# Kernel tuning notes

Hardware: AMD Instinct MI355X
Metric: run time of the kernel (lower is better)

## Reference

```python
import jax, jax.numpy as jnp
import numpy as np

B, S, E, F, R, T = 2, 2048, 768, 3072, 4, 128
H = 12  # num_heads
HD = E // H
HID = 128  # lora_mlp_dim


def _lin(key, out_f, in_f):
    bound = 1.0 / np.sqrt(in_f)
    return jax.random.uniform(key, (out_f, in_f), jnp.float32, -bound, bound)


def _bias(key, out_f, in_f):
    bound = 1.0 / np.sqrt(in_f)
    return jax.random.uniform(key, (out_f,), jnp.float32, -bound, bound)


def setup_inputs() -> dict:
    key = jax.random.key(0)
    ks = jax.random.split(key, 20)
    return {
        "src": jax.random.normal(ks[0], (B, S, E), jnp.float32),
        "task_embedding": jax.random.normal(ks[1], (B, S, T), jnp.float32),
        "norm1_w": jnp.ones((E,), jnp.float32),
        "norm2_w": jnp.ones((E,), jnp.float32),
        "in_proj_w": _lin(ks[2], 3 * E, E),      # MHA qkv, bias=False
        "out_proj_w": _lin(ks[3], E, E),          # MHA out, bias=False
        "ffn1_w": _lin(ks[4], F, E), "ffn1_b": _bias(ks[5], F, E),
        "ffn2_w": _lin(ks[6], E, F), "ffn2_b": _bias(ks[7], E, F),
        "hA_w1": _lin(ks[8], HID, T), "hA_b1": _bias(ks[9], HID, T),
        "hA_w2": _lin(ks[10], F * R, HID), "hA_b2": _bias(ks[11], F * R, HID),
        "hB_w1": _lin(ks[12], HID, T), "hB_b1": _bias(ks[13], HID, T),
        "hB_w2": _lin(ks[14], R * E, HID), "hB_b2": _bias(ks[15], R * E, HID),
    }


def _rmsnorm(x, w):
    eps = jnp.finfo(x.dtype).eps
    return x * jax.lax.rsqrt(jnp.mean(x * x, axis=-1, keepdims=True) + eps) * w


def reference(src, task_embedding, norm1_w, norm2_w, in_proj_w, out_proj_w,
              ffn1_w, ffn1_b, ffn2_w, ffn2_b,
              hA_w1, hA_b1, hA_w2, hA_b2, hB_w1, hB_b1, hB_w2, hB_b2):
    # --- self-attention block (pre-RMSNorm) ---
    x = _rmsnorm(src, norm1_w)
    qkv = jnp.einsum('bse,fe->bsf', x, in_proj_w)  # [B,S,3E]
    q, k, v = jnp.split(qkv, 3, axis=-1)
    q = q.reshape(B, S, H, HD).transpose(0, 2, 1, 3)
    k = k.reshape(B, S, H, HD).transpose(0, 2, 1, 3)
    v = v.reshape(B, S, H, HD).transpose(0, 2, 1, 3)
    scores = jnp.einsum('bhqd,bhkd->bhqk', q, k) / jnp.sqrt(jnp.float32(HD))
    attn = jax.nn.softmax(scores, axis=-1)
    ctx = jnp.einsum('bhqk,bhkd->bhqd', attn, v)
    ctx = ctx.transpose(0, 2, 1, 3).reshape(B, S, E)
    attn_out = jnp.einsum('bse,fe->bsf', ctx, out_proj_w)
    src = src + attn_out

    # --- FFN block with per-token hypernetwork LoRA on linear1 ---
    x = _rmsnorm(src, norm2_w)
    # hypernetwork: MLP(task) -> per-token A [F,R], B [R,E]
    hA = jax.nn.relu(jnp.einsum('bst,ht->bsh', task_embedding, hA_w1) + hA_b1)
    A_params = (jnp.einsum('bsh,fh->bsf', hA, hA_w2) + hA_b2).reshape(B, S, F, R)
    hB = jax.nn.relu(jnp.einsum('bst,ht->bsh', task_embedding, hB_w1) + hB_b1)
    B_params = (jnp.einsum('bsh,fh->bsf', hB, hB_w2) + hB_b2).reshape(B, S, R, E)

    base = jnp.einsum('bse,fe->bsf', x, ffn1_w) + ffn1_b  # [B,S,F]
    inter = jnp.einsum('bse,bsre->bsr', x, B_params)       # [B,S,R]
    adapt = jnp.einsum('bsr,bsfr->bsf', inter, A_params)   # [B,S,F]
    h = jax.nn.relu(base + adapt)
    out2 = jnp.einsum('bsf,ef->bse', h, ffn2_w) + ffn2_b
    return src + out2
```

## Files before the change

### kernel.cpp

```cpp
#include <hip/hip_runtime.h>
#include <math.h>

#define NB 2
#define NS 2048
#define NE 768
#define NF 3072
#define NHEAD 12
#define NTOK 4096
#define LDW 1344
#define VTS 2176

typedef __bf16 bf16;
typedef __bf16 bf16x2 __attribute__((ext_vector_type(2)));
typedef __bf16 bf16x4 __attribute__((ext_vector_type(4)));
typedef __bf16 bf16x8 __attribute__((ext_vector_type(8)));
typedef float  f32x4  __attribute__((ext_vector_type(4)));

__device__ __forceinline__ f32x4 mfma_bf16(bf16x8 a, bf16x8 b, f32x4 c) {
  return __builtin_amdgcn_mfma_f32_16x16x32_bf16(a, b, c, 0, 0, 0);
}

__device__ __forceinline__ float fast_exp2(float x) {
#if __has_builtin(__builtin_amdgcn_exp2f)
  return __builtin_amdgcn_exp2f(x);
#else
  return exp2f(x);
#endif
}

__device__ __forceinline__ void glds16(const void* g, void* l) {
  __builtin_amdgcn_global_load_lds((const __attribute__((address_space(1))) void*)g,
                                   (__attribute__((address_space(3))) void*)l,
                                   16, 0, 0);
}

__device__ __forceinline__ void pipe_barrier_keep4() {
  asm volatile("s_waitcnt vmcnt(4)" ::: "memory");
  __builtin_amdgcn_s_barrier();
  __builtin_amdgcn_sched_barrier(0);
}
__device__ __forceinline__ void pipe_barrier_drain() {
  asm volatile("s_waitcnt vmcnt(0)" ::: "memory");
  __builtin_amdgcn_s_barrier();
  __builtin_amdgcn_sched_barrier(0);
}

__device__ __forceinline__ void swz_xy(int& bx, int& by) {
  int gx = gridDim.x;
  int i = by*gx + bx;
  int xcd = i & 7, s = i >> 3;
  int bands = gridDim.y >> 3;
  by = xcd*bands + s / gx;
  bx = s % gx;
}

__global__ void prep_kernel(const float* __restrict__ in_proj, const float* __restrict__ out_proj,
                            const float* __restrict__ ffn1_w, const float* __restrict__ ffn1_b,
                            const float* __restrict__ ffn2_w,
                            const float* __restrict__ hA_w1, const float* __restrict__ hA_b1,
                            const float* __restrict__ hA_w2, const float* __restrict__ hA_b2,
                            const float* __restrict__ hB_w1, const float* __restrict__ hB_b1,
                            const float* __restrict__ hB_w2,
                            const float* __restrict__ task,
                            bf16* __restrict__ Wqkv, bf16* __restrict__ Wo, bf16* __restrict__ W2,
                            bf16* __restrict__ W1ab, float* __restrict__ b1ab,
                            bf16* __restrict__ WBp, bf16* __restrict__ Wc,
                            bf16* __restrict__ task_bf)
{
  __shared__ float tb[64*130];
  int stride = gridDim.x * blockDim.x;
  int t0 = blockIdx.x * blockDim.x + threadIdx.x;
  const float QS = 0.125f * 1.44269504088896f;
  for (int i = t0; i < (2304*768)/4; i += stride) {
    float4 v = ((const float4*)in_proj)[i];
    float sc = (i < (768*768)/4) ? QS : 1.0f;
    *(bf16x4*)(Wqkv + i*4) = (bf16x4){(bf16)(v.x*sc), (bf16)(v.y*sc), (bf16)(v.z*sc), (bf16)(v.w*sc)};
  }
  for (int i = t0; i < (768*768)/4; i += stride) {
    float4 v = ((const float4*)out_proj)[i];
    *(bf16x4*)(Wo + i*4) = (bf16x4){(bf16)v.x, (bf16)v.y, (bf16)v.z, (bf16)v.w};
  }
  for (int i = t0; i < (768*3072)/4; i += stride) {
    float4 v = ((const float4*)ffn2_w)[i];
    *(bf16x4*)(W2 + i*4) = (bf16x4){(bf16)v.x, (bf16)v.y, (bf16)v.z, (bf16)v.w};
  }
  for (int i = t0; i < (NTOK*128)/4; i += stride) {
    float4 v = ((const float4*)task)[i];
    *(bf16x4*)(task_bf + i*4) = (bf16x4){(bf16)v.x, (bf16)v.y, (bf16)v.z, (bf16)v.w};
  }
  for (int i = t0; i < 256*128;  i += stride)
    W1ab[i] = (bf16)(i < 128*128 ? hA_w1[i] : hB_w1[i - 128*128]);
  for (int i = t0; i < 256; i += stride) b1ab[i] = (i < 128) ? hA_b1[i] : hB_b1[i-128];

  for (int j0 = blockIdx.x*64; j0 < 3072; j0 += gridDim.x*64) {
    __syncthreads();
    for (int i = threadIdx.x; i < 64*128; i += 256) {
      int jr = i >> 7, hh = i & 127;
      tb[jr*130 + hh] = hB_w2[(long)(j0 + jr)*128 + hh];
    }
    __syncthreads();
    int r = j0 / 768, e0 = j0 % 768;
    for (int i = threadIdx.x; i < 128*64; i += 256) {
      int hh = i >> 6, jr = i & 63;
      WBp[(long)(r*128 + hh)*768 + e0 + jr] = (bf16)tb[jr*130 + hh];
    }
  }

  for (int f = blockIdx.x; f < 3072; f += gridDim.x) {
    const float* hrow = hA_w2 + (long)f*512;
    bf16* wrow = Wc + (long)f*LDW;
    for (int c = threadIdx.x; c < 768; c += 256) wrow[c] = (bf16)ffn1_w[(long)f*768 + c];
    for (int i = threadIdx.x; i < 512; i += 256) {
      int r = i >> 7, h = i & 127;
      wrow[768 + h*4 + r] = (bf16)hrow[i];
    }
    if (threadIdx.x < 4)        wrow[1280 + threadIdx.x] = (bf16)hA_b2[f*4 + threadIdx.x];
    else if (threadIdx.x == 4)  wrow[1284] = (bf16)ffn1_b[f];
    else if (threadIdx.x < 64)  wrow[1280 + threadIdx.x] = (bf16)0.f;
  }
}

__global__ __launch_bounds__(256) void rmsnorm_k(const float* __restrict__ x,
                                                 const float* __restrict__ w,
                                                 bf16* __restrict__ out, int ld_out)
{
  __shared__ float red[4];
  long t = blockIdx.x;
  const float* xr = x + t*NE;
  float ss = 0.f;
  #pragma unroll
  for (int i = 0; i < 3; i++) { float v = xr[threadIdx.x + i*256]; ss += v*v; }
  #pragma unroll
  for (int d = 1; d < 64; d <<= 1) ss += __shfl_xor(ss, d, 64);
  if ((threadIdx.x & 63) == 0) red[threadIdx.x >> 6] = ss;
  __syncthreads();
  float tot = red[0] + red[1] + red[2] + red[3];
  float scale = rsqrtf(tot * (1.f/768.f) + 1.1920928955078125e-07f);
  #pragma unroll
  for (int i = 0; i < 3; i++) {
    int idx = threadIdx.x + i*256;
    out[t*ld_out + idx] = (bf16)(xr[idx] * scale * w[idx]);
  }
}

__global__ __launch_bounds__(256, 2) void gemm_ph(const bf16* __restrict__ A,
                                                  const bf16* __restrict__ Bm,
                                                  bf16* __restrict__ C,
                                                  int nt, int lda, int ldb, int ldc)
{
  __shared__ bf16 As[2][2][128*32];
  __shared__ bf16 Bs[2][2][192*32];
  const int tid = threadIdx.x;
  int bx = blockIdx.x, by = blockIdx.y;
  swz_xy(bx, by);
  const int m0 = by * 128, n0 = bx * 192;
  const int w = tid >> 6, lane = tid & 63;
  const int quad = lane >> 4, l16 = lane & 15;
  const int wm = w >> 1, wn = w & 1;

  f32x4 acc[4][6];
  #pragma unroll
  for (int i = 0; i < 4; i++)
    #pragma unroll
    for (int j = 0; j < 6; j++) acc[i][j] = (f32x4){0.f,0.f,0.f,0.f};

  const int iA0 = tid,      RA0 = iA0 >> 3, cA0 = (iA0 & 7) ^ (RA0 & 7);
  const int iA1 = tid + 256,RA1 = iA1 >> 3, cA1 = (iA1 & 7) ^ (RA1 & 7);
  const int iB2 = tid + 512,RB2 = iB2 >> 3, cB2 = (iB2 & 7) ^ (RB2 & 7);
  const int rA0 = 2*RA0 + (cA0 >> 2), hA0c = (cA0 & 3)*8;
  const int rA1 = 2*RA1 + (cA1 >> 2), hA1c = (cA1 & 3)*8;
  const int rB2 = 2*RB2 + (cB2 >> 2), hB2c = (cB2 & 3)*8;
  const bf16* paA0 = A  + (long)(m0 + rA0)*lda + hA0c;
  const bf16* paA1 = A  + (long)(m0 + rA1)*lda + hA1c;
  const bf16* pbB0 = Bm + (long)(n0 + rA0)*ldb + hA0c;
  const bf16* pbB1 = Bm + (long)(n0 + rA1)*ldb + hA1c;
  const bf16* pbB2 = Bm + (long)(n0 + rB2)*ldb + hB2c;

  auto stageA = [&](int buf, int kh, int kt) {
    const int s = kt + kh*32;
    glds16(paA0 + s, (void*)(&As[buf][kh][tid*8]));
    glds16(paA1 + s, (void*)(&As[buf][kh][(tid + 256)*8]));
  };
  auto stageB = [&](int buf, int kh, int kt) {
    const int s = kt + kh*32;
    glds16(pbB0 + s, (void*)(&Bs[buf][kh][tid*8]));
    glds16(pbB1 + s, (void*)(&Bs[buf][kh][(tid + 256)*8]));
    glds16(pbB2 + s, (void*)(&Bs[buf][kh][(tid + 512)*8]));
  };

  const int Rh = l16 >> 1;
  const int jfr = (((l16 & 1) << 2) | quad) ^ Rh;
  const int aBase = wm*32, bBase = wn*48;

  auto barrier = [] { __builtin_amdgcn_s_barrier(); __builtin_amdgcn_sched_barrier(0); };

  stageA(0, 0, 0); stageB(0, 0, 0); stageA(0, 1, 0); stageB(0, 1, 0);
  asm volatile("s_waitcnt vmcnt(5)" ::: "memory");
  barrier();

  for (int t = 0; t < nt; ++t) {
    const int cur = t & 1, nb = cur ^ 1;
    const bool more = (t + 1 < nt);
    const int kt1 = (t + 1) << 6;
    bf16x8 af[2], bfr[6];

    #pragma unroll
    for (int j = 0; j < 2; ++j)
      af[j] = *(const bf16x8*)(&As[cur][0][(aBase + j*8 + Rh)*64 + jfr*8]);
    #pragma unroll
    for (int ni = 0; ni < 6; ++ni)
      bfr[ni] = *(const bf16x8*)(&Bs[cur][0][(bBase + ni*8 + Rh)*64 + jfr*8]);
    if (more) stageA(nb, 0, kt1);
    barrier();
    __builtin_amdgcn_s_setprio(1);
    #pragma unroll
    for (int j = 0; j < 2; ++j)
      #pragma unroll
      for (int ni = 0; ni < 6; ++ni)
        acc[j][ni] = mfma_bf16(af[j], bfr[ni], acc[j][ni]);
    __builtin_amdgcn_s_setprio(0);
    barrier();

    #pragma unroll
    for (int j = 0; j < 2; ++j)
      af[j] = *(const bf16x8*)(&As[cur][0][(aBase + 16 + j*8 + Rh)*64 + jfr*8]);
    if (more) stageB(nb, 0, kt1);
    barrier();
    __builtin_amdgcn_s_setprio(1);
    #pragma unroll
    for (int j = 0; j < 2; ++j)
      #pragma unroll
      for (int ni = 0; ni < 6; ++ni)
        acc[2 + j][ni] = mfma_bf16(af[j], bfr[ni], acc[2 + j][ni]);
    __builtin_amdgcn_s_setprio(0);
    if (more) asm volatile("s_waitcnt vmcnt(5)" ::: "memory");
    else      asm volatile("s_waitcnt vmcnt(0)" ::: "memory");
    barrier();

    #pragma unroll
    for (int j = 0; j < 2; ++j)
      af[j] = *(const bf16x8*)(&As[cur][1][(aBase + j*8 + Rh)*64 + jfr*8]);
    #pragma unroll
    for (int ni = 0; ni < 6; ++ni)
      bfr[ni] = *(const bf16x8*)(&Bs[cur][1][(bBase + ni*8 + Rh)*64 + jfr*8]);
    if (more) stageA(nb, 1, kt1);
    barrier();
    __builtin_amdgcn_s_setprio(1);
    #pragma unroll
    for (int j = 0; j < 2; ++j)
      #pragma unroll
      for (int ni = 0; ni < 6; ++ni)
        acc[j][ni] = mfma_bf16(af[j], bfr[ni], acc[j][ni]);
    __builtin_amdgcn_s_setprio(0);
    barrier();

    #pragma unroll
    for (int j = 0; j < 2; ++j)
      af[j] = *(const bf16x8*)(&As[cur][1][(aBase + 16 + j*8 + Rh)*64 + jfr*8]);
    if (more) stageB(nb, 1, kt1);
    barrier();
    __builtin_amdgcn_s_setprio(1);
    #pragma unroll
    for (int j = 0; j < 2; ++j)
      #pragma unroll
      for (int ni = 0; ni < 6; ++ni)
        acc[2 + j][ni] = mfma_bf16(af[j], bfr[ni], acc[2 + j][ni]);
    __builtin_amdgcn_s_setprio(0);
    if (more) asm volatile("s_waitcnt vmcnt(5)" ::: "memory");
    barrier();
  }

  #pragma unroll
  for (int mi = 0; mi < 4; ++mi)
    #pragma unroll
    for (int ni = 0; ni < 6; ++ni) {
      int col = n0 + wn*96 + ni*16 + l16;
      #pragma unroll
      for (int r = 0; r < 4; ++r) {
        long row = m0 + wm*64 + mi*16 + quad*4 + r;
        float v = acc[mi][ni][r];
        C[row*ldc + col] = (bf16)(v > 0.f ? v : 0.f);
      }
    }
}

template<typename OutT, bool RELU, bool BIAS, bool RES>
__global__ __launch_bounds__(256) void gemm64(const bf16* __restrict__ A,
                                              const bf16* __restrict__ Bm,
                                              OutT* __restrict__ C,
                                              const float* __restrict__ bias,
                                              const float* __restrict__ res,
                                              int K, int lda, int ldb, int ldc)
{
  __shared__ bf16 As[3][64*64];
  __shared__ bf16 Bs[3][64*64];
  const int tid = threadIdx.x;
  int bx = blockIdx.x, by = blockIdx.y;
  swz_xy(bx, by);
  const int m0 = by * 64, n0 = bx * 64;
  const int w = tid >> 6, lane = tid & 63;
  const int quad = lane >> 4, l16 = lane & 15;
  const int wy = w >> 1, wx = w & 1;
  const int sw = l16 & 7;

  f32x4 acc[2][2];
  #pragma unroll
  for (int i = 0; i < 2; i++)
    #pragma unroll
    for (int j = 0; j < 2; j++) acc[i][j] = (f32x4){0.f,0.f,0.f,0.f};

  const int c0 = tid, c1 = tid + 256;
  const int r0 = c0 >> 3, g0 = ((c0 & 7) ^ (r0 & 7)) * 8;
  const int r1 = c1 >> 3, g1 = ((c1 & 7) ^ (r1 & 7)) * 8;
  const bf16* pA0 = A  + (long)(m0 + r0)*lda + g0;
  const bf16* pA1 = A  + (long)(m0 + r1)*lda + g1;
  const bf16* pB0 = Bm + (long)(n0 + r0)*ldb + g0;
  const bf16* pB1 = Bm + (long)(n0 + r1)*ldb + g1;
  auto stage = [&](int buf) {
    glds16(pA0, (void*)(&As[buf][c0*8]));
    glds16(pA1, (void*)(&As[buf][c1*8]));
    glds16(pB0, (void*)(&Bs[buf][c0*8]));
    glds16(pB1, (void*)(&Bs[buf][c1*8]));
    pA0 += 64; pA1 += 64; pB0 += 64; pB1 += 64;
  };

  const int nsteps = K >> 6;
  stage(0);
  if (nsteps > 1) stage(1);
  pipe_barrier_keep4();

  int cur = 0, nx2 = 2;
  for (int s = 0; s < nsteps; ++s) {
    const bool more = (s + 2 < nsteps);
    if (more) stage(nx2);

    bf16x8 af[2][2], bfr[2][2];
    #pragma unroll
    for (int mi = 0; mi < 2; ++mi)
      #pragma unroll
      for (int kb = 0; kb < 2; ++kb)
        af[mi][kb] = *(const bf16x8*)(&As[cur][(wy*32 + mi*16 + l16)*64 + (((kb*4 + quad) ^ sw))*8]);
    #pragma unroll
    for (int ni = 0; ni < 2; ++ni)
      #pragma unroll
      for (int kb = 0; kb < 2; ++kb)
        bfr[ni][kb] = *(const bf16x8*)(&Bs[cur][(wx*32 + ni*16 + l16)*64 + (((kb*4 + quad) ^ sw))*8]);
    #pragma unroll
    for (int kb = 0; kb < 2; ++kb)
      #pragma unroll
      for (int mi = 0; mi < 2; ++mi)
        #pragma unroll
        for (int ni = 0; ni < 2; ++ni)
          acc[mi][ni] = mfma_bf16(af[mi][kb], bfr[ni][kb], acc[mi][ni]);

    if (more) pipe_barrier_keep4();
    else      pipe_barrier_drain();
    cur = (cur == 2) ? 0 : cur + 1;
    nx2 = (nx2 == 2) ? 0 : nx2 + 1;
  }

  #pragma unroll
  for (int mi = 0; mi < 2; ++mi)
    #pragma unroll
    for (int ni = 0; ni < 2; ++ni) {
      int col = n0 + wx*32 + ni*16 + l16;
      #pragma unroll
      for (int r = 0; r < 4; ++r) {
        long row = m0 + wy*32 + mi*16 + quad*4 + r;
        float v = acc[mi][ni][r];
        if (BIAS) v += bias[col];
        if (RES)  v += res[row*ldc + col];
        if (RELU) v = v > 0.f ? v : 0.f;
        C[row*ldc + col] = (OutT)v;
      }
    }
}

__global__ __launch_bounds__(256) void gemm_qkv64(const bf16* __restrict__ A,
                                                  const bf16* __restrict__ Bm,
                                                  bf16* __restrict__ Qkv,
                                                  bf16* __restrict__ Vt)
{
  __shared__ bf16 As[3][64*64];
  __shared__ bf16 Bs[3][64*64];
  const int tid = threadIdx.x;
  int bx = blockIdx.x, by = blockIdx.y;
  swz_xy(bx, by);
  const int m0 = by * 64, n0 = bx * 64;
  const int w = tid >> 6, lane = tid & 63;
  const int quad = lane >> 4, l16 = lane & 15;
  const int wy = w >> 1, wx = w & 1;
  const int sw = l16 & 7;

  f32x4 acc[2][2];
  #pragma unroll
  for (int i = 0; i < 2; i++)
    #pragma unroll
    for (int j = 0; j < 2; j++) acc[i][j] = (f32x4){0.f,0.f,0.f,0.f};

  const int c0 = tid, c1 = tid + 256;
  const int r0 = c0 >> 3, g0 = ((c0 & 7) ^ (r0 & 7)) * 8;
  const int r1 = c1 >> 3, g1 = ((c1 & 7) ^ (r1 & 7)) * 8;
  const bf16* pA0 = A  + (long)(m0 + r0)*768 + g0;
  const bf16* pA1 = A  + (long)(m0 + r1)*768 + g1;
  const bf16* pB0 = Bm + (long)(n0 + r0)*768 + g0;
  const bf16* pB1 = Bm + (long)(n0 + r1)*768 + g1;
  auto stage = [&](int buf) {
    glds16(pA0, (void*)(&As[buf][c0*8]));
    glds16(pA1, (void*)(&As[buf][c1*8]));
    glds16(pB0, (void*)(&Bs[buf][c0*8]));
    glds16(pB1, (void*)(&Bs[buf][c1*8]));
    pA0 += 64; pA1 += 64; pB0 += 64; pB1 += 64;
  };

  stage(0);
  stage(1);
  pipe_barrier_keep4();

  int cur = 0, nx2 = 2;
  for (int s = 0; s < 12; ++s) {
    const bool more = (s + 2 < 12);
    if (more) stage(nx2);

    bf16x8 af[2][2], bfr[2][2];
    #pragma unroll
    for (int mi = 0; mi < 2; ++mi)
      #pragma unroll
      for (int kb = 0; kb < 2; ++kb)
        af[mi][kb] = *(const bf16x8*)(&As[cur][(wy*32 + mi*16 + l16)*64 + (((kb*4 + quad) ^ sw))*8]);
    #pragma unroll
    for (int ni = 0; ni < 2; ++ni)
      #pragma unroll
      for (int kb = 0; kb < 2; ++kb)
        bfr[ni][kb] = *(const bf16x8*)(&Bs[cur][(wx*32 + ni*16 + l16)*64 + (((kb*4 + quad) ^ sw))*8]);
    #pragma unroll
    for (int kb = 0; kb < 2; ++kb)
      #pragma unroll
      for (int mi = 0; mi < 2; ++mi)
        #pragma unroll
        for (int ni = 0; ni < 2; ++ni)
          acc[mi][ni] = mfma_bf16(af[mi][kb], bfr[ni][kb], acc[mi][ni]);

    if (more) pipe_barrier_keep4();
    else      pipe_barrier_drain();
    cur = (cur == 2) ? 0 : cur + 1;
    nx2 = (nx2 == 2) ? 0 : nx2 + 1;
  }

  const int bb = m0 >> 11;
  #pragma unroll
  for (int mi = 0; mi < 2; ++mi)
    #pragma unroll
    for (int ni = 0; ni < 2; ++ni) {
      int col = n0 + wx*32 + ni*16 + l16;
      #pragma unroll
      for (int r = 0; r < 4; ++r) {
        long row = m0 + wy*32 + mi*16 + quad*4 + r;
        bf16 v = (bf16)acc[mi][ni][r];
        if (col < 1536) {
          Qkv[row*2304 + col] = v;
        } else {
          int vc = col - 1536;
          int hh = vc >> 6, d = vc & 63;
          long srow = row & (NS-1);
          Vt[((long)(bb*NHEAD + hh)*64 + d)*VTS + srow] = v;
        }
      }
    }
}

__global__ __launch_bounds__(256, 2) void flash_attn(const bf16* __restrict__ Qkv,
                                                     const bf16* __restrict__ Vt,
                                                     bf16* __restrict__ Ctx)
{
  __shared__ bf16 Ks[2][2][64*64];
  __shared__ bf16 Vs[2][2][64*64];

  const int tid = threadIdx.x;
  const int w = tid >> 6, lane = tid & 63;
  const int quad = lane >> 4, l16 = lane & 15;
  const int pair = w >> 1, qw = w & 1;
  int bx = blockIdx.x, by = blockIdx.y;
  swz_xy(bx, by);
  const int bh = by;
  const int b = bh / NHEAD, h = bh % NHEAD;
  const int q0 = bx * 64;

  bf16x8 qf[2][2];
  #pragma unroll
  for (int mi = 0; mi < 2; ++mi) {
    const long tq = (long)(b*NS + q0 + qw*32 + mi*16 + l16);
    qf[mi][0] = *(const bf16x8*)(Qkv + tq*2304 + h*64 + quad*8);
    qf[mi][1] = *(const bf16x8*)(Qkv + tq*2304 + h*64 + 32 + quad*8);
  }

  bf16x8 ones;
  #pragma unroll
  for (int j = 0; j < 8; ++j) ones[j] = (bf16)1.0f;

  f32x4 o[2][4];
  f32x4 o5[2];
  #pragma unroll
  for (int mi = 0; mi < 2; ++mi) {
    o5[mi] = (f32x4){0.f,0.f,0.f,0.f};
    #pragma unroll
    for (int i = 0; i < 4; i++) o[mi][i] = (f32x4){0.f,0.f,0.f,0.f};
  }

  const int ptid = tid & 127;
  const bf16* kp[4];
  const bf16* vp[4];
  int cc[4];
  #pragma unroll
  for (int i = 0; i < 4; ++i) {
    int c = ptid + i*128;
    cc[i] = c;
    int r = c >> 3, g = ((c & 7) ^ (r & 7)) * 8;
    kp[i] = Qkv + (long)(b*NS + pair*1024 + r)*2304 + 768 + h*64 + g;
    vp[i] = Vt + ((long)bh*64 + r)*VTS + pair*1024 + g;
  }
  auto stage = [&](int buf) {
    #pragma unroll
    for (int i = 0; i < 4; ++i) {
      glds16(kp[i], (void*)(&Ks[pair][buf][cc[i]*8]));
      glds16(vp[i], (void*)(&Vs[pair][buf][cc[i]*8]));
      kp[i] += (long)64*2304; vp[i] += 64;
    }
  };

  auto body = [&](int cur) {
    bf16x8 kfr[4][2];
    #pragma unroll
    for (int nt = 0; nt < 4; ++nt)
      #pragma unroll
      for (int kb = 0; kb < 2; ++kb)
        kfr[nt][kb] = *(const bf16x8*)(&Ks[pair][cur][(nt*16 + l16)*64 + (((kb*4 + quad) ^ (l16 & 7)))*8]);

    bf16x8 pf[2][2];
    #pragma unroll
    for (int mi = 0; mi < 2; ++mi) {
      f32x4 s[4];
      #pragma unroll
      for (int nt = 0; nt < 4; ++nt) {
        s[nt] = (f32x4){0.f,0.f,0.f,0.f};
        #pragma unroll
        for (int kb = 0; kb < 2; ++kb)
          s[nt] = mfma_bf16(kfr[nt][kb], qf[mi][kb], s[nt]);
      }
      #pragma unroll
      for (int nt = 0; nt < 4; ++nt)
        #pragma unroll
        for (int r = 0; r < 4; ++r)
          pf[mi][nt >> 1][(nt & 1)*4 + r] = (bf16)fast_exp2(s[nt][r]);
    }
    #pragma unroll
    for (int ntp = 0; ntp < 2; ++ntp) {
      bf16x8 vf[4];
      #pragma unroll
      for (int dt = 0; dt < 4; ++dt) {
        int row = dt*16 + l16;
        int cA = ntp*4 + (quad >> 1);
        int base = row*64 + (quad & 1)*4;
        bf16x4 va = *(const bf16x4*)(&Vs[pair][cur][base + ((cA       ^ (row & 7)) << 3)]);
        bf16x4 vb = *(const bf16x4*)(&Vs[pair][cur][base + (((cA + 2) ^ (row & 7)) << 3)]);
        vf[dt] = (bf16x8){va[0],va[1],va[2],va[3], vb[0],vb[1],vb[2],vb[3]};
      }
      #pragma unroll
      for (int mi = 0; mi < 2; ++mi) {
        #pragma unroll
        for (int dt = 0; dt < 4; ++dt)
          o[mi][dt] = mfma_bf16(pf[mi][ntp], vf[dt], o[mi][dt]);
        o5[mi] = mfma_bf16(pf[mi][ntp], ones, o5[mi]);
      }
    }
  };

  stage(0);
  __builtin_amdgcn_s_waitcnt(0);
  __syncthreads();

  for (int t = 0; t < 16; t += 2) {
    stage(1);
    body(0);
    __builtin_amdgcn_s_waitcnt(0);
    __syncthreads();
    if (t + 2 < 16) stage(0);
    body(1);
    __builtin_amdgcn_s_waitcnt(0);
    __syncthreads();
  }

  float* Of = (float*)&Ks[0][0][0];
  float* Lf = Of + 64*68;
  const int rbase = qw*32;
  if (pair == 1) {
    #pragma unroll
    for (int mi = 0; mi < 2; ++mi)
      #pragma unroll
      for (int r = 0; r < 4; ++r) {
        int row = rbase + mi*16 + quad*4 + r;
        if (l16 == 0) Lf[row] = o5[mi][r];
        #pragma unroll
        for (int dt = 0; dt < 4; ++dt)
          Of[row*68 + dt*16 + l16] = o[mi][dt][r];
      }
  }
  __syncthreads();
  if (pair == 0) {
    #pragma unroll
    for (int mi = 0; mi < 2; ++mi)
      #pragma unroll
      for (int r = 0; r < 4; ++r) {
        int row = rbase + mi*16 + quad*4 + r;
        float inv = 1.f / (o5[mi][r] + Lf[row]);
        long trow = (long)(b*NS + q0 + row);
        #pragma unroll
        for (int dt = 0; dt < 4; ++dt)
          Ctx[trow*NE + h*64 + dt*16 + l16] =
            (bf16)((o[mi][dt][r] + Of[row*68 + dt*16 + l16]) * inv);
      }
  }
}

__global__ __launch_bounds__(256) void build_g(const bf16* __restrict__ HAB,
                                               const float* __restrict__ P,
                                               const float* __restrict__ hB_b2,
                                               bf16* __restrict__ Aext)
{
  long t = blockIdx.x*4 + (threadIdx.x >> 6);
  int lane = threadIdx.x & 63;
  const bf16* xr = Aext + t*LDW;
  float acc[4] = {0.f, 0.f, 0.f, 0.f};
  #pragma unroll
  for (int k = 0; k < 6; ++k) {
    int idx = lane + k*64;
    bf16x2 xv = *(const bf16x2*)(xr + idx*2);
    float x0 = (float)xv[0], x1 = (float)xv[1];
    #pragma unroll
    for (int r = 0; r < 4; ++r)
      acc[r] += x0 * hB_b2[r*768 + idx*2] + x1 * hB_b2[r*768 + idx*2 + 1];
  }
  const bf16* hB = HAB + t*256 + 128;
  const float* Pr = P + t*512;
  #pragma unroll
  for (int k = 0; k < 2; ++k) {
    int h = lane + k*64;
    float hv = (float)hB[h];
    #pragma unroll
    for (int r = 0; r < 4; ++r) acc[r] += hv * Pr[r*128 + h];
  }
  #pragma unroll
  for (int r = 0; r < 4; ++r)
    #pragma unroll
    for (int d = 1; d < 64; d <<= 1) acc[r] += __shfl_xor(acc[r], d, 64);

  bf16* grow = Aext + t*LDW + 768;
  const bf16* hA = HAB + t*256;
  bf16x8 gv;
  #pragma unroll
  for (int j = 0; j < 8; ++j) {
    int idx = lane*8 + j;
    int h = idx >> 2, r = idx & 3;
    gv[j] = (bf16)((float)hA[h] * acc[r]);
  }
  *(bf16x8*)(grow + lane*8) = gv;
  if (lane < 4)       Aext[t*LDW + 1280 + lane] = (bf16)acc[lane];
  else if (lane == 4) Aext[t*LDW + 1284] = (bf16)1.0f;
  else                Aext[t*LDW + 1280 + lane] = (bf16)0.f;
}

extern "C" void kernel_launch(void* const* d_in, const int* in_sizes, int n_in,
                              void* d_out, int out_size, void* d_ws, size_t ws_size,
                              hipStream_t stream)
{
  const float* src      = (const float*)d_in[0];
  const float* task     = (const float*)d_in[1];
  const float* norm1_w  = (const float*)d_in[2];
  const float* norm2_w  = (const float*)d_in[3];
  const float* in_proj  = (const float*)d_in[4];
  const float* out_proj = (const float*)d_in[5];
  const float* ffn1_w   = (const float*)d_in[6];
  const float* ffn1_b   = (const float*)d_in[7];
  const float* ffn2_w   = (const float*)d_in[8];
  const float* ffn2_b   = (const float*)d_in[9];
  const float* hA_w1    = (const float*)d_in[10];
  const float* hA_b1    = (const float*)d_in[11];
  const float* hA_w2    = (const float*)d_in[12];
  const float* hA_b2    = (const float*)d_in[13];
  const float* hB_w1    = (const float*)d_in[14];
  const float* hB_b1    = (const float*)d_in[15];
  const float* hB_w2    = (const float*)d_in[16];
  const float* hB_b2    = (const float*)d_in[17];
  float* out = (float*)d_out;

  char* ws = (char*)d_ws;
  size_t off = 0;
  auto alloc = [&](size_t bytes) { size_t o = off; off += (bytes + 255) & ~(size_t)255; return o; };
  bf16*  Wqkv   = (bf16*)(ws + alloc(2304*768*2));
  bf16*  Wo     = (bf16*)(ws + alloc(768*768*2));
  bf16*  W2     = (bf16*)(ws + alloc(768*3072*2));
  bf16*  W1ab   = (bf16*)(ws + alloc(256*128*2));
  float* b1ab   = (float*)(ws + alloc(256*4));
  bf16*  WBp    = (bf16*)(ws + alloc(512*768*2));
  bf16*  Wc     = (bf16*)(ws + alloc((size_t)3072*LDW*2));
  bf16*  taskbf = (bf16*)(ws + alloc((size_t)NTOK*128*2));
  bf16*  XC     = (bf16*)(ws + alloc((size_t)NTOK*768*2));
  char*  QKVH   = ws + alloc(25559040);
  bf16*  Qkv    = (bf16*)QKVH;
  bf16*  Vt     = (bf16*)(QKVH + 18874368);
  bf16*  Hbuf   = (bf16*)QKVH;
  float* Src2   = (float*)(ws + alloc((size_t)NTOK*768*4));
  bf16*  Aext   = (bf16*)(ws + alloc((size_t)NTOK*LDW*2));
  bf16*  HAB    = (bf16*)(ws + alloc((size_t)NTOK*256*2));
  float* P      = (float*)(ws + alloc((size_t)NTOK*512*4));

  prep_kernel<<<dim3(1280), 256, 0, stream>>>(in_proj, out_proj, ffn1_w, ffn1_b, ffn2_w,
      hA_w1, hA_b1, hA_w2, hA_b2, hB_w1, hB_b1, hB_w2, task,
      Wqkv, Wo, W2, W1ab, b1ab, WBp, Wc, taskbf);
  rmsnorm_k<<<dim3(NTOK), 256, 0, stream>>>(src, norm1_w, XC, 768);
  gemm_qkv64<<<dim3(36,64), 256, 0, stream>>>(XC, Wqkv, Qkv, Vt);
  flash_attn<<<dim3(32,24), 256, 0, stream>>>(Qkv, Vt, XC);
  gemm64<float,false,false,true><<<dim3(12,64), 256, 0, stream>>>(XC, Wo, Src2, nullptr, src, 768, 768, 768, 768);
  rmsnorm_k<<<dim3(NTOK), 256, 0, stream>>>(Src2, norm2_w, Aext, LDW);
  gemm64<bf16,true,true,false><<<dim3(4,64), 256, 0, stream>>>(taskbf, W1ab, HAB, b1ab, nullptr, 128, 128, 128, 256);
  gemm64<float,false,false,false><<<dim3(8,64), 256, 0, stream>>>(Aext, WBp, P, nullptr, nullptr, 768, LDW, 768, 512);
  build_g<<<dim3(NTOK/4), 256, 0, stream>>>(HAB, P, hB_b2, Aext);
  gemm_ph<<<dim3(16,32), 256, 0, stream>>>(Aext, Wc, Hbuf, 21, LDW, LDW, 3072);
  gemm64<float,false,true,true><<<dim3(12,64), 256, 0, stream>>>(Hbuf, W2, out, ffn2_b, Src2, 3072, 3072, 3072, 768);
}
```

Before: 205.1 us.

## Enlarge LoRA-fused FFN1 GEMM tile to 256x192 with 512-thread blocks

The FFN1+LoRA GEMM now uses 256x192 output tiles computed by 8 waves in a 2x4 layout, instead of 128x192 tiles with 4 waves. This halves the number of blocks, so each block reuses its B tile across twice as many rows and redundant B traffic drops. The B tile for both K halves is now staged in one pass, and the vmcnt waits are adjusted to match. The cost is more LDS per block (about 112KB), which likely limits residency to one block per CU, and each wave now reads more A fragments per step.

```diff
diff --git a/kernel.cpp b/kernel.cpp
--- a/kernel.cpp
+++ b/kernel.cpp
@@ -143,141 +143,145 @@
   }
 }
 
-__global__ __launch_bounds__(256, 2) void gemm_ph(const bf16* __restrict__ A,
-                                                  const bf16* __restrict__ Bm,
-                                                  bf16* __restrict__ C,
-                                                  int nt, int lda, int ldb, int ldc)
+__global__ __launch_bounds__(512, 2) void gemm_ph256(const bf16* __restrict__ A,
+                                                     const bf16* __restrict__ Bm,
+                                                     bf16* __restrict__ C,
+                                                     int nt, int lda, int ldb, int ldc)
 {
-  __shared__ bf16 As[2][2][128*32];
+  __shared__ bf16 As[2][2][256*32];
   __shared__ bf16 Bs[2][2][192*32];
   const int tid = threadIdx.x;
   int bx = blockIdx.x, by = blockIdx.y;
   swz_xy(bx, by);
-  const int m0 = by * 128, n0 = bx * 192;
+  const int m0 = by * 256, n0 = bx * 192;
   const int w = tid >> 6, lane = tid & 63;
   const int quad = lane >> 4, l16 = lane & 15;
-  const int wm = w >> 1, wn = w & 1;
-
-  f32x4 acc[4][6];
-  #pragma unroll
-  for (int i = 0; i < 4; i++)
-    #pragma unroll
-    for (int j = 0; j < 6; j++) acc[i][j] = (f32x4){0.f,0.f,0.f,0.f};
-
-  const int iA0 = tid,      RA0 = iA0 >> 3, cA0 = (iA0 & 7) ^ (RA0 & 7);
-  const int iA1 = tid + 256,RA1 = iA1 >> 3, cA1 = (iA1 & 7) ^ (RA1 & 7);
-  const int iB2 = tid + 512,RB2 = iB2 >> 3, cB2 = (iB2 & 7) ^ (RB2 & 7);
-  const int rA0 = 2*RA0 + (cA0 >> 2), hA0c = (cA0 & 3)*8;
-  const int rA1 = 2*RA1 + (cA1 >> 2), hA1c = (cA1 & 3)*8;
-  const int rB2 = 2*RB2 + (cB2 >> 2), hB2c = (cB2 & 3)*8;
-  const bf16* paA0 = A  + (long)(m0 + rA0)*lda + hA0c;
-  const bf16* paA1 = A  + (long)(m0 + rA1)*lda + hA1c;
-  const bf16* pbB0 = Bm + (long)(n0 + rA0)*ldb + hA0c;
-  const bf16* pbB1 = Bm + (long)(n0 + rA1)*ldb + hA1c;
-  const bf16* pbB2 = Bm + (long)(n0 + rB2)*ldb + hB2c;
+  const int wm = w >> 2, wn = w & 3;
+
+  f32x4 acc[8][3];
+  #pragma unroll
+  for (int i = 0; i < 8; i++)
+    #pragma unroll
+    for (int j = 0; j < 3; j++) acc[i][j] = (f32x4){0.f,0.f,0.f,0.f};
+
+  const int cA0 = tid, cA1 = tid + 512;
+  const int RA0 = cA0 >> 3, xA0 = (cA0 & 7) ^ (RA0 & 7);
+  const int RA1 = cA1 >> 3, xA1 = (cA1 & 7) ^ (RA1 & 7);
+  const bf16* paA0 = A + (long)(m0 + 2*RA0 + (xA0 >> 2))*lda + (xA0 & 3)*8;
+  const bf16* paA1 = A + (long)(m0 + 2*RA1 + (xA1 >> 2))*lda + (xA1 & 3)*8;
+
+  const bf16* pbB[3];
+  int bofs[3];
+  #pragma unroll
+  for (int i = 0; i < 3; ++i) {
+    int c = tid + i*512;
+    int kh = c / 768, cc = c - kh*768;
+    int R = cc >> 3, cx = (cc & 7) ^ (R & 7);
+    int row = 2*R + (cx >> 2), col8 = (cx & 3)*8;
+    pbB[i] = Bm + (long)(n0 + row)*ldb + kh*32 + col8;
+    bofs[i] = kh*(192*32) + cc*8;
+  }
 
   auto stageA = [&](int buf, int kh, int kt) {
-    const int s = kt + kh*32;
-    glds16(paA0 + s, (void*)(&As[buf][kh][tid*8]));
-    glds16(paA1 + s, (void*)(&As[buf][kh][(tid + 256)*8]));
+    glds16(paA0 + kt + kh*32, (void*)(&As[buf][kh][cA0*8]));
+    glds16(paA1 + kt + kh*32, (void*)(&As[buf][kh][cA1*8]));
   };
-  auto stageB = [&](int buf, int kh, int kt) {
-    const int s = kt + kh*32;
-    glds16(pbB0 + s, (void*)(&Bs[buf][kh][tid*8]));
-    glds16(pbB1 + s, (void*)(&Bs[buf][kh][(tid + 256)*8]));
-    glds16(pbB2 + s, (void*)(&Bs[buf][kh][(tid + 512)*8]));
+  auto stageB = [&](int buf, int kt) {
+    bf16* base = &Bs[buf][0][0];
+    #pragma unroll
+    for (int i = 0; i < 3; ++i)
+      glds16(pbB[i] + kt, (void*)(base + bofs[i]));
   };
 
   const int Rh = l16 >> 1;
   const int jfr = (((l16 & 1) << 2) | quad) ^ Rh;
-  const int aBase = wm*32, bBase = wn*48;
+  const int aBase = wm*64, bBase = wn*24;
 
   auto barrier = [] { __builtin_amdgcn_s_barrier(); __builtin_amdgcn_sched_barrier(0); };
 
-  stageA(0, 0, 0); stageB(0, 0, 0); stageA(0, 1, 0); stageB(0, 1, 0);
-  asm volatile("s_waitcnt vmcnt(5)" ::: "memory");
+  stageA(0, 0, 0); stageB(0, 0); stageA(0, 1, 0);
+  asm volatile("s_waitcnt vmcnt(2)" ::: "memory");
   barrier();
 
   for (int t = 0; t < nt; ++t) {
     const int cur = t & 1, nb = cur ^ 1;
     const bool more = (t + 1 < nt);
     const int kt1 = (t + 1) << 6;
-    bf16x8 af[2], bfr[6];
-
-    #pragma unroll
-    for (int j = 0; j < 2; ++j)
+    bf16x8 af[4], bfr[3];
+
+    #pragma unroll
+    for (int j = 0; j < 4; ++j)
       af[j] = *(const bf16x8*)(&As[cur][0][(aBase + j*8 + Rh)*64 + jfr*8]);
     #pragma unroll
-    for (int ni = 0; ni < 6; ++ni)
+    for (int ni = 0; ni < 3; ++ni)
       bfr[ni] = *(const bf16x8*)(&Bs[cur][0][(bBase + ni*8 + Rh)*64 + jfr*8]);
     if (more) stageA(nb, 0, kt1);
     barrier();
     __builtin_amdgcn_s_setprio(1);
     #pragma unroll
-    for (int j = 0; j < 2; ++j)
-      #pragma unroll
-      for (int ni = 0; ni < 6; ++ni)
+    for (int j = 0; j < 4; ++j)
+      #pragma unroll
+      for (int ni = 0; ni < 3; ++ni)
         acc[j][ni] = mfma_bf16(af[j], bfr[ni], acc[j][ni]);
     __builtin_amdgcn_s_setprio(0);
     barrier();
 
     #pragma unroll
-    for (int j = 0; j < 2; ++j)
-      af[j] = *(const bf16x8*)(&As[cur][0][(aBase + 16 + j*8 + Rh)*64 + jfr*8]);
-    if (more) stageB(nb, 0, kt1);
+    for (int j = 0; j < 4; ++j)
+      af[j] = *(const bf16x8*)(&As[cur][0][(aBase + 32 + j*8 + Rh)*64 + jfr*8]);
+    if (more) stageB(nb, kt1);
     barrier();
     __builtin_amdgcn_s_setprio(1);
     #pragma unroll
-    for (int j = 0; j < 2; ++j)
-      #pragma unroll
-      for (int ni = 0; ni < 6; ++ni)
-        acc[2 + j][ni] = mfma_bf16(af[j], bfr[ni], acc[2 + j][ni]);
+    for (int j = 0; j < 4; ++j)
+      #pragma unroll
+      for (int ni = 0; ni < 3; ++ni)
+        acc[4 + j][ni] = mfma_bf16(af[j], bfr[ni], acc[4 + j][ni]);
     __builtin_amdgcn_s_setprio(0);
     if (more) asm volatile("s_waitcnt vmcnt(5)" ::: "memory");
     else      asm volatile("s_waitcnt vmcnt(0)" ::: "memory");
     barrier();
 
     #pragma unroll
-    for (int j = 0; j < 2; ++j)
+    for (int j = 0; j < 4; ++j)
       af[j] = *(const bf16x8*)(&As[cur][1][(aBase + j*8 + Rh)*64 + jfr*8]);
     #pragma unroll
-    for (int ni = 0; ni < 6; ++ni)
+    for (int ni = 0; ni < 3; ++ni)
       bfr[ni] = *(const bf16x8*)(&Bs[cur][1][(bBase + ni*8 + Rh)*64 + jfr*8]);
     if (more) stageA(nb, 1, kt1);
     barrier();
     __builtin_amdgcn_s_setprio(1);
     #pragma unroll
-    for (int j = 0; j < 2; ++j)
-      #pragma unroll
-      for (int ni = 0; ni < 6; ++ni)
+    for (int j = 0; j < 4; ++j)
+      #pragma unroll
+      for (int ni = 0; ni < 3; ++ni)
         acc[j][ni] = mfma_bf16(af[j], bfr[ni], acc[j][ni]);
     __builtin_amdgcn_s_setprio(0);
     barrier();
 
     #pragma unroll
-    for (int j = 0; j < 2; ++j)
-      af[j] = *(const bf16x8*)(&As[cur][1][(aBase + 16 + j*8 + Rh)*64 + jfr*8]);
-    if (more) stageB(nb, 1, kt1);
+    for (int j = 0; j < 4; ++j)
+      af[j] = *(const bf16x8*)(&As[cur][1][(aBase + 32 + j*8 + Rh)*64 + jfr*8]);
     barrier();
     __builtin_amdgcn_s_setprio(1);
     #pragma unroll
-    for (int j = 0; j < 2; ++j)
-      #pragma unroll
-      for (int ni = 0; ni < 6; ++ni)
-        acc[2 + j][ni] = mfma_bf16(af[j], bfr[ni], acc[2 + j][ni]);
+    for (int j = 0; j < 4; ++j)
+      #pragma unroll
+      for (int ni = 0; ni < 3; ++ni)
+        acc[4 + j][ni] = mfma_bf16(af[j], bfr[ni], acc[4 + j][ni]);
     __builtin_amdgcn_s_setprio(0);
-    if (more) asm volatile("s_waitcnt vmcnt(5)" ::: "memory");
+    if (more) asm volatile("s_waitcnt vmcnt(2)" ::: "memory");
     barrier();
   }
 
   #pragma unroll
-  for (int mi = 0; mi < 4; ++mi)
-    #pragma unroll
-    for (int ni = 0; ni < 6; ++ni) {
-      int col = n0 + wn*96 + ni*16 + l16;
+  for (int mi = 0; mi < 8; ++mi)
+    #pragma unroll
+    for (int ni = 0; ni < 3; ++ni) {
+      int col = n0 + wn*48 + ni*16 + l16;
       #pragma unroll
       for (int r = 0; r < 4; ++r) {
-        long row = m0 + wm*64 + mi*16 + quad*4 + r;
+        long row = m0 + wm*128 + mi*16 + quad*4 + r;
         float v = acc[mi][ni][r];
         C[row*ldc + col] = (bf16)(v > 0.f ? v : 0.f);
       }
@@ -725,6 +729,6 @@
   gemm64<bf16,true,true,false><<<dim3(4,64), 256, 0, stream>>>(taskbf, W1ab, HAB, b1ab, nullptr, 128, 128, 128, 256);
   gemm64<float,false,false,false><<<dim3(8,64), 256, 0, stream>>>(Aext, WBp, P, nullptr, nullptr, 768, LDW, 768, 512);
   build_g<<<dim3(NTOK/4), 256, 0, stream>>>(HAB, P, hB_b2, Aext);
-  gemm_ph<<<dim3(16,32), 256, 0, stream>>>(Aext, Wc, Hbuf, 21, LDW, LDW, 3072);
+  gemm_ph256<<<dim3(16,16), 512, 0, stream>>>(Aext, Wc, Hbuf, 21, LDW, LDW, 3072);
   gemm64<float,false,true,true><<<dim3(12,64), 256, 0, stream>>>(Hbuf, W2, out, ffn2_b, Src2, 3072, 3072, 3072, 768);
 }
```

After: 207.5 us. About the same (+1.1%).

## Replace 64x64 QKV GEMM with 128x192 phased-pipeline tile kernel

Applied to the files above, without the earlier changes.

Replaces the 64x64-tile QKV projection GEMM with a 128x192-tile kernel. It copies the gemm_ph phased structure: double-buffered K halves, global-to-LDS loads interleaved between MFMA phases, and s_setprio around the MFMAs. Each wave now computes a 64x96 output, which raises data reuse and cuts LDS and global traffic per FLOP. The grid shrinks from 2304 to 384 blocks, about 1.5 waves on 256 CUs, so some tail imbalance is possible.

```diff
diff --git a/kernel.cpp b/kernel.cpp
--- a/kernel.cpp
+++ b/kernel.cpp
@@ -284,6 +284,156 @@
     }
 }
 
+__global__ __launch_bounds__(256, 2) void gemm_ph_qkv(const bf16* __restrict__ A,
+                                                      const bf16* __restrict__ Bm,
+                                                      bf16* __restrict__ Qkv,
+                                                      bf16* __restrict__ Vt)
+{
+  __shared__ bf16 As[2][2][128*32];
+  __shared__ bf16 Bs[2][2][192*32];
+  const int tid = threadIdx.x;
+  int bx = blockIdx.x, by = blockIdx.y;
+  swz_xy(bx, by);
+  const int m0 = by * 128, n0 = bx * 192;
+  const int w = tid >> 6, lane = tid & 63;
+  const int quad = lane >> 4, l16 = lane & 15;
+  const int wm = w >> 1, wn = w & 1;
+  const int lda = 768, ldb = 768, nt = 12;
+
+  f32x4 acc[4][6];
+  #pragma unroll
+  for (int i = 0; i < 4; i++)
+    #pragma unroll
+    for (int j = 0; j < 6; j++) acc[i][j] = (f32x4){0.f,0.f,0.f,0.f};
+
+  const int iA0 = tid,      RA0 = iA0 >> 3, cA0 = (iA0 & 7) ^ (RA0 & 7);
+  const int iA1 = tid + 256,RA1 = iA1 >> 3, cA1 = (iA1 & 7) ^ (RA1 & 7);
+  const int iB2 = tid + 512,RB2 = iB2 >> 3, cB2 = (iB2 & 7) ^ (RB2 & 7);
+  const int rA0 = 2*RA0 + (cA0 >> 2), hA0c = (cA0 & 3)*8;
+  const int rA1 = 2*RA1 + (cA1 >> 2), hA1c = (cA1 & 3)*8;
+  const int rB2 = 2*RB2 + (cB2 >> 2), hB2c = (cB2 & 3)*8;
+  const bf16* paA0 = A  + (long)(m0 + rA0)*lda + hA0c;
+  const bf16* paA1 = A  + (long)(m0 + rA1)*lda + hA1c;
+  const bf16* pbB0 = Bm + (long)(n0 + rA0)*ldb + hA0c;
+  const bf16* pbB1 = Bm + (long)(n0 + rA1)*ldb + hA1c;
+  const bf16* pbB2 = Bm + (long)(n0 + rB2)*ldb + hB2c;
+
+  auto stageA = [&](int buf, int kh, int kt) {
+    const int s = kt + kh*32;
+    glds16(paA0 + s, (void*)(&As[buf][kh][tid*8]));
+    glds16(paA1 + s, (void*)(&As[buf][kh][(tid + 256)*8]));
+  };
+  auto stageB = [&](int buf, int kh, int kt) {
+    const int s = kt + kh*32;
+    glds16(pbB0 + s, (void*)(&Bs[buf][kh][tid*8]));
+    glds16(pbB1 + s, (void*)(&Bs[buf][kh][(tid + 256)*8]));
+    glds16(pbB2 + s, (void*)(&Bs[buf][kh][(tid + 512)*8]));
+  };
+
+  const int Rh = l16 >> 1;
+  const int jfr = (((l16 & 1) << 2) | quad) ^ Rh;
+  const int aBase = wm*32, bBase = wn*48;
+
+  auto barrier = [] { __builtin_amdgcn_s_barrier(); __builtin_amdgcn_sched_barrier(0); };
+
+  stageA(0, 0, 0); stageB(0, 0, 0); stageA(0, 1, 0); stageB(0, 1, 0);
+  asm volatile("s_waitcnt vmcnt(5)" ::: "memory");
+  barrier();
+
+  for (int t = 0; t < nt; ++t) {
+    const int cur = t & 1, nb = cur ^ 1;
+    const bool more = (t + 1 < nt);
+    const int kt1 = (t + 1) << 6;
+    bf16x8 af[2], bfr[6];
+
+    #pragma unroll
+    for (int j = 0; j < 2; ++j)
+      af[j] = *(const bf16x8*)(&As[cur][0][(aBase + j*8 + Rh)*64 + jfr*8]);
+    #pragma unroll
+    for (int ni = 0; ni < 6; ++ni)
+      bfr[ni] = *(const bf16x8*)(&Bs[cur][0][(bBase + ni*8 + Rh)*64 + jfr*8]);
+    if (more) stageA(nb, 0, kt1);
+    barrier();
+    __builtin_amdgcn_s_setprio(1);
+    #pragma unroll
+    for (int j = 0; j < 2; ++j)
+      #pragma unroll
+      for (int ni = 0; ni < 6; ++ni)
+        acc[j][ni] = mfma_bf16(af[j], bfr[ni], acc[j][ni]);
+    __builtin_amdgcn_s_setprio(0);
+    barrier();
+
+    #pragma unroll
+    for (int j = 0; j < 2; ++j)
+      af[j] = *(const bf16x8*)(&As[cur][0][(aBase + 16 + j*8 + Rh)*64 + jfr*8]);
+    if (more) stageB(nb, 0, kt1);
+    barrier();
+    __builtin_amdgcn_s_setprio(1);
+    #pragma unroll
+    for (int j = 0; j < 2; ++j)
+      #pragma unroll
+      for (int ni = 0; ni < 6; ++ni)
+        acc[2 + j][ni] = mfma_bf16(af[j], bfr[ni], acc[2 + j][ni]);
+    __builtin_amdgcn_s_setprio(0);
+    if (more) asm volatile("s_waitcnt vmcnt(5)" ::: "memory");
+    else      asm volatile("s_waitcnt vmcnt(0)" ::: "memory");
+    barrier();
+
+    #pragma unroll
+    for (int j = 0; j < 2; ++j)
+      af[j] = *(const bf16x8*)(&As[cur][1][(aBase + j*8 + Rh)*64 + jfr*8]);
+    #pragma unroll
+    for (int ni = 0; ni < 6; ++ni)
+      bfr[ni] = *(const bf16x8*)(&Bs[cur][1][(bBase + ni*8 + Rh)*64 + jfr*8]);
+    if (more) stageA(nb, 1, kt1);
+    barrier();
+    __builtin_amdgcn_s_setprio(1);
+    #pragma unroll
+    for (int j = 0; j < 2; ++j)
+      #pragma unroll
+      for (int ni = 0; ni < 6; ++ni)
+        acc[j][ni] = mfma_bf16(af[j], bfr[ni], acc[j][ni]);
+    __builtin_amdgcn_s_setprio(0);
+    barrier();
+
+    #pragma unroll
+    for (int j = 0; j < 2; ++j)
+      af[j] = *(const bf16x8*)(&As[cur][1][(aBase + 16 + j*8 + Rh)*64 + jfr*8]);
+    if (more) stageB(nb, 1, kt1);
+    barrier();
+    __builtin_amdgcn_s_setprio(1);
+    #pragma unroll
+    for (int j = 0; j < 2; ++j)
+      #pragma unroll
+      for (int ni = 0; ni < 6; ++ni)
+        acc[2 + j][ni] = mfma_bf16(af[j], bfr[ni], acc[2 + j][ni]);
+    __builtin_amdgcn_s_setprio(0);
+    if (more) asm volatile("s_waitcnt vmcnt(5)" ::: "memory");
+    barrier();
+  }
+
+  #pragma unroll
+  for (int mi = 0; mi < 4; ++mi)
+    #pragma unroll
+    for (int ni = 0; ni < 6; ++ni) {
+      int col = n0 + wn*96 + ni*16 + l16;
+      #pragma unroll
+      for (int r = 0; r < 4; ++r) {
+        long row = m0 + wm*64 + mi*16 + quad*4 + r;
+        bf16 v = (bf16)acc[mi][ni][r];
+        if (col < 1536) {
+          Qkv[row*2304 + col] = v;
+        } else {
+          int vc = col - 1536;
+          int hh = vc >> 6, d = vc & 63;
+          long bb = row >> 11;
+          long srow = row & (NS-1);
+          Vt[((bb*NHEAD + hh)*64 + d)*VTS + srow] = v;
+        }
+      }
+    }
+}
+
 template<typename OutT, bool RELU, bool BIAS, bool RES>
 __global__ __launch_bounds__(256) void gemm64(const bf16* __restrict__ A,
                                               const bf16* __restrict__ Bm,
@@ -372,99 +522,6 @@
         if (RES)  v += res[row*ldc + col];
         if (RELU) v = v > 0.f ? v : 0.f;
         C[row*ldc + col] = (OutT)v;
-      }
-    }
-}
-
-__global__ __launch_bounds__(256) void gemm_qkv64(const bf16* __restrict__ A,
-                                                  const bf16* __restrict__ Bm,
-                                                  bf16* __restrict__ Qkv,
-                                                  bf16* __restrict__ Vt)
-{
-  __shared__ bf16 As[3][64*64];
-  __shared__ bf16 Bs[3][64*64];
-  const int tid = threadIdx.x;
-  int bx = blockIdx.x, by = blockIdx.y;
-  swz_xy(bx, by);
-  const int m0 = by * 64, n0 = bx * 64;
-  const int w = tid >> 6, lane = tid & 63;
-  const int quad = lane >> 4, l16 = lane & 15;
-  const int wy = w >> 1, wx = w & 1;
-  const int sw = l16 & 7;
-
-  f32x4 acc[2][2];
-  #pragma unroll
-  for (int i = 0; i < 2; i++)
-    #pragma unroll
-    for (int j = 0; j < 2; j++) acc[i][j] = (f32x4){0.f,0.f,0.f,0.f};
-
-  const int c0 = tid, c1 = tid + 256;
-  const int r0 = c0 >> 3, g0 = ((c0 & 7) ^ (r0 & 7)) * 8;
-  const int r1 = c1 >> 3, g1 = ((c1 & 7) ^ (r1 & 7)) * 8;
-  const bf16* pA0 = A  + (long)(m0 + r0)*768 + g0;
-  const bf16* pA1 = A  + (long)(m0 + r1)*768 + g1;
-  const bf16* pB0 = Bm + (long)(n0 + r0)*768 + g0;
-  const bf16* pB1 = Bm + (long)(n0 + r1)*768 + g1;
-  auto stage = [&](int buf) {
-    glds16(pA0, (void*)(&As[buf][c0*8]));
-    glds16(pA1, (void*)(&As[buf][c1*8]));
-    glds16(pB0, (void*)(&Bs[buf][c0*8]));
-    glds16(pB1, (void*)(&Bs[buf][c1*8]));
-    pA0 += 64; pA1 += 64; pB0 += 64; pB1 += 64;
-  };
-
-  stage(0);
-  stage(1);
-  pipe_barrier_keep4();
-
-  int cur = 0, nx2 = 2;
-  for (int s = 0; s < 12; ++s) {
-    const bool more = (s + 2 < 12);
-    if (more) stage(nx2);
-
-    bf16x8 af[2][2], bfr[2][2];
-    #pragma unroll
-    for (int mi = 0; mi < 2; ++mi)
-      #pragma unroll
-      for (int kb = 0; kb < 2; ++kb)
-        af[mi][kb] = *(const bf16x8*)(&As[cur][(wy*32 + mi*16 + l16)*64 + (((kb*4 + quad) ^ sw))*8]);
-    #pragma unroll
-    for (int ni = 0; ni < 2; ++ni)
-      #pragma unroll
-      for (int kb = 0; kb < 2; ++kb)
-        bfr[ni][kb] = *(const bf16x8*)(&Bs[cur][(wx*32 + ni*16 + l16)*64 + (((kb*4 + quad) ^ sw))*8]);
-    #pragma unroll
-    for (int kb = 0; kb < 2; ++kb)
-      #pragma unroll
-      for (int mi = 0; mi < 2; ++mi)
-        #pragma unroll
-        for (int ni = 0; ni < 2; ++ni)
-          acc[mi][ni] = mfma_bf16(af[mi][kb], bfr[ni][kb], acc[mi][ni]);
-
-    if (more) pipe_barrier_keep4();
-    else      pipe_barrier_drain();
-    cur = (cur == 2) ? 0 : cur + 1;
-    nx2 = (nx2 == 2) ? 0 : nx2 + 1;
-  }
-
-  const int bb = m0 >> 11;
-  #pragma unroll
-  for (int mi = 0; mi < 2; ++mi)
-    #pragma unroll
-    for (int ni = 0; ni < 2; ++ni) {
-      int col = n0 + wx*32 + ni*16 + l16;
-      #pragma unroll
-      for (int r = 0; r < 4; ++r) {
-        long row = m0 + wy*32 + mi*16 + quad*4 + r;
-        bf16 v = (bf16)acc[mi][ni][r];
-        if (col < 1536) {
-          Qkv[row*2304 + col] = v;
-        } else {
-          int vc = col - 1536;
-          int hh = vc >> 6, d = vc & 63;
-          long srow = row & (NS-1);
-          Vt[((long)(bb*NHEAD + hh)*64 + d)*VTS + srow] = v;
-        }
       }
     }
 }
@@ -718,7 +775,7 @@
       hA_w1, hA_b1, hA_w2, hA_b2, hB_w1, hB_b1, hB_w2, task,
       Wqkv, Wo, W2, W1ab, b1ab, WBp, Wc, taskbf);
   rmsnorm_k<<<dim3(NTOK), 256, 0, stream>>>(src, norm1_w, XC, 768);
-  gemm_qkv64<<<dim3(36,64), 256, 0, stream>>>(XC, Wqkv, Qkv, Vt);
+  gemm_ph_qkv<<<dim3(12,32), 256, 0, stream>>>(XC, Wqkv, Qkv, Vt);
   flash_attn<<<dim3(32,24), 256, 0, stream>>>(Qkv, Vt, XC);
   gemm64<float,false,false,true><<<dim3(12,64), 256, 0, stream>>>(XC, Wo, Src2, nullptr, src, 768, 768, 768, 768);
   rmsnorm_k<<<dim3(NTOK), 256, 0, stream>>>(Src2, norm2_w, Aext, LDW);
```

After: 205.3 us. About the same (+0.1%).
